# Optimization experiments

Measured on AMD Instinct MI355X. Metric: run time of the kernel, lower is better.

## Reference

```python
import jax, jax.numpy as jnp
import numpy as np

RECEPTIVE_FIELD = 3  # padding radius r; number of shifts = (2r+1)^2 = 49


def setup_inputs() -> dict:
    key = jax.random.key(0)
    image = jax.random.normal(key, (16, 3, 384, 384), dtype=jnp.float32)
    return {"image": image}


def reference(image):
    r = RECEPTIVE_FIELD
    B, C, H, W = image.shape
    # Pad with +inf, constant mode (torchvision.transforms.Pad(fill=inf))
    padded = jnp.pad(image, ((0, 0), (0, 0), (r, r), (r, r)),
                     mode="constant", constant_values=jnp.inf)
    # Unfold with kernel (H, W) over the padded image enumerates (2r+1)^2
    # shifted HxW windows in row-major (dy, dx) order. For each shift,
    # absolute color distance summed over the 3 channels (cost volume).
    k = 2 * r + 1
    g = jnp.stack(
        [jnp.abs(image - jax.lax.dynamic_slice(padded, (0, 0, dy, dx), (B, C, H, W))).sum(axis=1)
         for dy in range(k) for dx in range(k)],
        axis=1,
    )  # [B, (2r+1)^2, H, W]
    # Original replaces NaNs with inf (inf-padded border artifacts)
    g = jnp.where(jnp.isnan(g), jnp.inf, g)
    return jnp.squeeze(g)
```

## Files before the change

### kernel.cpp

```cpp
#include <hip/hip_runtime.h>
#include <math.h>

#define RF   3
#define KK   7
#define NS   49
#define HH   384
#define WW   384
#define BB   16
#define CC   3
#define HW   (HH*WW)

#define TX   32
#define TY   8
#define PXW  4
#define TILE_W (TX*PXW)
#define TILE_H (TY)
#define LXR  (TILE_W + 2*RF)
#define LX   136
#define LY   (TILE_H + 2*RF)

#define BIG_FINITE 1.0e38f

__global__ __launch_bounds__(TX*TY)
void cost_volume_kernel(const float* __restrict__ img, float* __restrict__ out)
{
    __shared__ float lds[CC][LY][LX];

    const int b      = blockIdx.z;
    const int tile_x = blockIdx.x * TILE_W;
    const int tile_y = blockIdx.y * TILE_H;
    const int tx     = threadIdx.x;
    const int ty     = threadIdx.y;
    const int tid    = ty * TX + tx;

    const float INF = __builtin_inff();

    const int total = CC * LY * LX;
    for (int i = tid; i < total; i += TX*TY) {
        int c   = i / (LY * LX);
        int rem = i - c * (LY * LX);
        int ly  = rem / LX;
        int lx  = rem - ly * LX;
        int gy  = tile_y + ly - RF;
        int gx  = tile_x + lx - RF;
        float v = INF;
        if (gy >= 0 && gy < HH && gx >= 0 && gx < WW && lx < LXR)
            v = img[(((size_t)b * CC + c) * HH + gy) * WW + gx];
        lds[c][ly][lx] = v;
    }
    __syncthreads();


    float cen[CC][PXW];
    {
        #pragma unroll
        for (int c = 0; c < CC; ++c) {
            const float4* rp = (const float4*)&lds[c][ty + RF][PXW*tx];
            float4 t0 = rp[0], t1 = rp[1];
            cen[c][0] = t0.w;
            cen[c][1] = t1.x;
            cen[c][2] = t1.y;
            cen[c][3] = t1.z;
        }
    }

    const int y0 = tile_y + ty;
    const int x0 = tile_x + PXW*tx;
    float* base = out + ((size_t)b * NS) * HW + (size_t)y0 * WW + x0;

    #pragma unroll
    for (int dy = 0; dy < KK; ++dy) {
        float wf[CC][12];
        #pragma unroll
        for (int c = 0; c < CC; ++c) {
            const float4* rp = (const float4*)&lds[c][ty + dy][PXW*tx];
            float4 t0 = rp[0], t1 = rp[1], t2 = rp[2];
            wf[c][0]=t0.x; wf[c][1]=t0.y; wf[c][2]=t0.z;  wf[c][3]=t0.w;
            wf[c][4]=t1.x; wf[c][5]=t1.y; wf[c][6]=t1.z;  wf[c][7]=t1.w;
            wf[c][8]=t2.x; wf[c][9]=t2.y; wf[c][10]=t2.z; wf[c][11]=t2.w;
        }
        #pragma unroll
        for (int dx = 0; dx < KK; ++dx) {
            float g[PXW];
            #pragma unroll
            for (int j = 0; j < PXW; ++j) {
                float s = 0.f;
                #pragma unroll
                for (int c = 0; c < CC; ++c)
                    s += fabsf(cen[c][j] - wf[c][dx + j]);
                g[j] = fminf(s, BIG_FINITE);
            }
            float4 res = make_float4(g[0], g[1], g[2], g[3]);
            *(float4*)(base + (size_t)(dy*KK + dx) * HW) = res;
        }
    }
}

extern "C" void kernel_launch(void* const* d_in, const int* in_sizes, int n_in,
                              void* d_out, int out_size, void* d_ws, size_t ws_size,
                              hipStream_t stream)
{
    const float* img = (const float*)d_in[0];
    float* out       = (float*)d_out;

    dim3 grid(WW / TILE_W, HH / TILE_H, BB);
    dim3 block(TX, TY, 1);
    cost_volume_kernel<<<grid, block, 0, stream>>>(img, out);
}
```

Baseline: 114.6 us.

## Tile by full-width row strips to cut horizontal halo reloads

Each block now covers a full-width strip of 8 rows across the 384-column image, using 384 threads that each handle two 4-pixel chunks. The previous 128x8 tiles loaded a 3-pixel horizontal halo on both sides. Full-width strips drop that redundant halo traffic and reduce the block count. In exchange, the LDS footprint per block grows and there are fewer, larger blocks, which can affect occupancy and load balance across CUs.

Result: slower. 142.7 us (+24.5%).

```diff
diff --git a/kernel.cpp b/kernel.cpp
--- a/kernel.cpp
+++ b/kernel.cpp
@@ -10,88 +10,84 @@
 #define CC   3
 #define HW   (HH*WW)
 
-#define TX   32
-#define TY   8
-#define PXW  4
-#define TILE_W (TX*PXW)
-#define TILE_H (TY)
-#define LXR  (TILE_W + 2*RF)
-#define LX   136
-#define LY   (TILE_H + 2*RF)
+#define SH    8
+#define NTH   384
+#define LY    (SH + 2*RF)
+#define LXP   392
+#define NCHUNK (SH*WW/4)
+#define CPT   (NCHUNK/NTH)
 
 #define BIG_FINITE 1.0e38f
 
-__global__ __launch_bounds__(TX*TY)
+__global__ __launch_bounds__(NTH)
 void cost_volume_kernel(const float* __restrict__ img, float* __restrict__ out)
 {
-    __shared__ float lds[CC][LY][LX];
+    __shared__ float lds[CC][LY][LXP];
 
-    const int b      = blockIdx.z;
-    const int tile_x = blockIdx.x * TILE_W;
-    const int tile_y = blockIdx.y * TILE_H;
-    const int tx     = threadIdx.x;
-    const int ty     = threadIdx.y;
-    const int tid    = ty * TX + tx;
+    const int strip = blockIdx.x;
+    const int b     = blockIdx.y;
+    const int y0    = strip * SH;
+    const int tid   = threadIdx.x;
 
     const float INF = __builtin_inff();
 
-    const int total = CC * LY * LX;
-    for (int i = tid; i < total; i += TX*TY) {
-        int c   = i / (LY * LX);
-        int rem = i - c * (LY * LX);
-        int ly  = rem / LX;
-        int lx  = rem - ly * LX;
-        int gy  = tile_y + ly - RF;
-        int gx  = tile_x + lx - RF;
+    const int total = CC * LY * LXP;
+    for (int i = tid; i < total; i += NTH) {
+        int c   = i / (LY * LXP);
+        int rem = i - c * (LY * LXP);
+        int ly  = rem / LXP;
+        int lx  = rem - ly * LXP;
+        int gy  = y0 + ly - RF;
+        int gx  = lx - RF;
         float v = INF;
-        if (gy >= 0 && gy < HH && gx >= 0 && gx < WW && lx < LXR)
+        if (gy >= 0 && gy < HH && gx >= 0 && gx < WW)
             v = img[(((size_t)b * CC + c) * HH + gy) * WW + gx];
         lds[c][ly][lx] = v;
     }
     __syncthreads();
 
+    #pragma unroll
+    for (int q = 0; q < CPT; ++q) {
+        const int ch  = tid + q * NTH;
+        const int row = ch / (WW / 4);
+        const int x0  = (ch - row * (WW / 4)) * 4;
 
-    float cen[CC][PXW];
-    {
+        float cen[CC][4];
         #pragma unroll
         for (int c = 0; c < CC; ++c) {
-            const float4* rp = (const float4*)&lds[c][ty + RF][PXW*tx];
+            const float4* rp = (const float4*)&lds[c][row + RF][x0];
             float4 t0 = rp[0], t1 = rp[1];
-            cen[c][0] = t0.w;
-            cen[c][1] = t1.x;
-            cen[c][2] = t1.y;
-            cen[c][3] = t1.z;
+            cen[c][0] = t0.w; cen[c][1] = t1.x;
+            cen[c][2] = t1.y; cen[c][3] = t1.z;
         }
-    }
 
-    const int y0 = tile_y + ty;
-    const int x0 = tile_x + PXW*tx;
-    float* base = out + ((size_t)b * NS) * HW + (size_t)y0 * WW + x0;
+        float* pbase = out + ((size_t)b * NS) * HW + (size_t)(y0 + row) * WW + x0;
 
-    #pragma unroll
-    for (int dy = 0; dy < KK; ++dy) {
-        float wf[CC][12];
         #pragma unroll
-        for (int c = 0; c < CC; ++c) {
-            const float4* rp = (const float4*)&lds[c][ty + dy][PXW*tx];
-            float4 t0 = rp[0], t1 = rp[1], t2 = rp[2];
-            wf[c][0]=t0.x; wf[c][1]=t0.y; wf[c][2]=t0.z;  wf[c][3]=t0.w;
-            wf[c][4]=t1.x; wf[c][5]=t1.y; wf[c][6]=t1.z;  wf[c][7]=t1.w;
-            wf[c][8]=t2.x; wf[c][9]=t2.y; wf[c][10]=t2.z; wf[c][11]=t2.w;
-        }
-        #pragma unroll
-        for (int dx = 0; dx < KK; ++dx) {
-            float g[PXW];
+        for (int dy = 0; dy < KK; ++dy) {
+            float wf[CC][12];
             #pragma unroll
-            for (int j = 0; j < PXW; ++j) {
-                float s = 0.f;
+            for (int c = 0; c < CC; ++c) {
+                const float4* rp = (const float4*)&lds[c][row + dy][x0];
+                float4 t0 = rp[0], t1 = rp[1], t2 = rp[2];
+                wf[c][0]=t0.x; wf[c][1]=t0.y; wf[c][2]=t0.z;  wf[c][3]=t0.w;
+                wf[c][4]=t1.x; wf[c][5]=t1.y; wf[c][6]=t1.z;  wf[c][7]=t1.w;
+                wf[c][8]=t2.x; wf[c][9]=t2.y; wf[c][10]=t2.z; wf[c][11]=t2.w;
+            }
+            #pragma unroll
+            for (int dx = 0; dx < KK; ++dx) {
+                float g[4];
                 #pragma unroll
-                for (int c = 0; c < CC; ++c)
-                    s += fabsf(cen[c][j] - wf[c][dx + j]);
-                g[j] = fminf(s, BIG_FINITE);
+                for (int j = 0; j < 4; ++j) {
+                    float s = 0.f;
+                    #pragma unroll
+                    for (int c = 0; c < CC; ++c)
+                        s += fabsf(cen[c][j] - wf[c][dx + j]);
+                    g[j] = fminf(s, BIG_FINITE);
+                }
+                *(float4*)(pbase + (size_t)(dy * KK + dx) * HW) =
+                    make_float4(g[0], g[1], g[2], g[3]);
             }
-            float4 res = make_float4(g[0], g[1], g[2], g[3]);
-            *(float4*)(base + (size_t)(dy*KK + dx) * HW) = res;
         }
     }
 }
@@ -103,7 +99,7 @@
     const float* img = (const float*)d_in[0];
     float* out       = (float*)d_out;
 
-    dim3 grid(WW / TILE_W, HH / TILE_H, BB);
-    dim3 block(TX, TY, 1);
+    dim3 grid(HH / SH, BB, 1);
+    dim3 block(NTH, 1, 1);
     cost_volume_kernel<<<grid, block, 0, stream>>>(img, out);
 }
```
